# Kernel tuning notes

Hardware: AMD Instinct MI355X
Metric: run time of the kernel (lower is better)

The kernel has to match this reference:

```python
import jax, jax.numpy as jnp
import numpy as np

NEG_SLOPE = 0.01
H = 128  # hidden_conv_1 == hidden_conv_2


def leaky(x):
    return jnp.where(x >= 0, x, NEG_SLOPE * x)


def gru_cell(x, h, w_ih, w_hh, b_ih, b_hh):
    # PyTorch GRUCell: gates stacked [r, z, n] along dim 0 of w_ih/w_hh
    gi = x @ w_ih.T + b_ih  # [N, 3H]
    gh = h @ w_hh.T + b_hh
    ir, iz, inn = jnp.split(gi, 3, axis=-1)
    hr, hz, hn = jnp.split(gh, 3, axis=-1)
    r = jax.nn.sigmoid(ir + hr)
    z = jax.nn.sigmoid(iz + hz)
    n = jnp.tanh(inn + r * hn)
    return (1.0 - z) * n + z * h


def gcn_conv(x, w, b, src, dst, num_nodes):
    # PyG GCNConv: add self-loops, symmetric normalization, linear first
    xw = x @ w.T  # [N, H]
    loop = jnp.arange(num_nodes, dtype=src.dtype)
    s = jnp.concatenate([src, loop])
    d = jnp.concatenate([dst, loop])
    deg = jax.ops.segment_sum(jnp.ones_like(d, dtype=x.dtype), d, num_segments=num_nodes)
    dinv = jnp.where(deg > 0, jax.lax.rsqrt(deg), 0.0)
    norm = dinv[s] * dinv[d]  # [E+N]
    msg = xw[s] * norm[:, None]
    out = jax.ops.segment_sum(msg, d, num_segments=num_nodes)
    return out + b


def setup_inputs() -> dict:
    key = jax.random.key(0)
    ks = jax.random.split(key, 24)
    N, E, EL, IN_DIM, OUT_DIM = 100000, 600000, 200000, 128, 2

    def lin(k, fan_in, fan_out):
        k1, k2 = jax.random.split(k)
        bound = 1.0 / np.sqrt(fan_in)
        w = jax.random.uniform(k1, (fan_out, fan_in), minval=-bound, maxval=bound, dtype=jnp.float32)
        b = jax.random.uniform(k2, (fan_out,), minval=-bound, maxval=bound, dtype=jnp.float32)
        return w, b

    w_pre1, b_pre1 = lin(ks[0], IN_DIM, 256)
    w_pre2, b_pre2 = lin(ks[1], 256, H)
    w_c1, b_c1 = lin(ks[2], H, H)
    w_c2, b_c2 = lin(ks[3], H, H)
    w_post, b_post = lin(ks[4], H, OUT_DIM)

    def gru_params(k):
        k1, k2, k3, k4 = jax.random.split(k, 4)
        bound = 1.0 / np.sqrt(H)
        u = lambda kk, shape: jax.random.uniform(kk, shape, minval=-bound, maxval=bound, dtype=jnp.float32)
        return u(k1, (3 * H, H)), u(k2, (3 * H, H)), u(k3, (3 * H,)), u(k4, (3 * H,))

    g1_wih, g1_whh, g1_bih, g1_bhh = gru_params(ks[5])
    g2_wih, g2_whh, g2_bih, g2_bhh = gru_params(ks[6])

    x = jax.random.normal(ks[7], (N, IN_DIM), dtype=jnp.float32)
    edge_index = jax.random.randint(ks[8], (2, E), 0, N, dtype=jnp.int64 if jax.config.jax_enable_x64 else jnp.int32)
    edge_label_index = jax.random.randint(ks[9], (2, EL), 0, N, dtype=edge_index.dtype)
    prev_emb0 = jax.random.normal(ks[10], (N, H), dtype=jnp.float32)
    prev_emb1 = jax.random.normal(ks[11], (N, H), dtype=jnp.float32)

    return {
        'x': x, 'edge_index': edge_index, 'edge_label_index': edge_label_index,
        'prev_emb0': prev_emb0, 'prev_emb1': prev_emb1,
        'w_pre1': w_pre1, 'b_pre1': b_pre1, 'w_pre2': w_pre2, 'b_pre2': b_pre2,
        'w_c1': w_c1, 'b_c1': b_c1, 'w_c2': w_c2, 'b_c2': b_c2,
        'w_post': w_post, 'b_post': b_post,
        'g1_wih': g1_wih, 'g1_whh': g1_whh, 'g1_bih': g1_bih, 'g1_bhh': g1_bhh,
        'g2_wih': g2_wih, 'g2_whh': g2_whh, 'g2_bih': g2_bih, 'g2_bhh': g2_bhh,
    }


def reference(x, edge_index, edge_label_index, prev_emb0, prev_emb1,
              w_pre1, b_pre1, w_pre2, b_pre2, w_c1, b_c1, w_c2, b_c2,
              w_post, b_post, g1_wih, g1_whh, g1_bih, g1_bhh,
              g2_wih, g2_whh, g2_bih, g2_bhh):
    N = x.shape[0]
    src, dst = edge_index[0], edge_index[1]

    # preprocess (dropout p=0.0 -> identity)
    h = leaky(x @ w_pre1.T + b_pre1)
    h = leaky(h @ w_pre2.T + b_pre2)

    # unconditional GRU fuse with previous 0-hop embedding (detached in torch)
    h = jax.lax.stop_gradient(gru_cell(h, prev_emb0, g1_wih, g1_whh, g1_bih, g1_bhh))
    emb0 = h

    h = leaky(gcn_conv(h, w_c1, b_c1, src, dst, N))
    h = jax.lax.stop_gradient(gru_cell(h, prev_emb0, g1_wih, g1_whh, g1_bih, g1_bhh))
    emb1 = h

    h = leaky(gcn_conv(h, w_c2, b_c2, src, dst, N))
    h = jax.lax.stop_gradient(gru_cell(h, prev_emb1, g2_wih, g2_whh, g2_bih, g2_bhh))
    emb2 = h

    # LP head: gather + hadamard + linear + sum
    h_src = h[edge_label_index[0]]
    h_dst = h[edge_label_index[1]]
    logits = jnp.sum((h_src * h_dst) @ w_post.T + b_post, axis=-1)  # [EL]
    return logits, emb0, emb1, emb2
```

## Files before the change

### kernel.cpp

```cpp
#include <hip/hip_runtime.h>
#include <hip/hip_bf16.h>
#include <type_traits>


typedef __bf16 bf16;
typedef __bf16 bf16x8 __attribute__((ext_vector_type(8)));
typedef float  f32x4  __attribute__((ext_vector_type(4)));

#define DEV __device__ __forceinline__

DEV f32x4 mfma16(bf16x8 a, bf16x8 b, f32x4 c) {
    return __builtin_amdgcn_mfma_f32_16x16x32_bf16(a, b, c, 0, 0, 0);
}

DEV bf16x8 load_a8(const float* p) {
    f32x4 lo = *(const f32x4*)p;
    f32x4 hi = *(const f32x4*)(p + 4);
    bf16x8 v;
    v[0] = (bf16)lo[0]; v[1] = (bf16)lo[1]; v[2] = (bf16)lo[2]; v[3] = (bf16)lo[3];
    v[4] = (bf16)hi[0]; v[5] = (bf16)hi[1]; v[6] = (bf16)hi[2]; v[7] = (bf16)hi[3];
    return v;
}
DEV bf16x8 load_a8(const bf16* p) { return *(const bf16x8*)p; }

__global__ void cvt8_kernel(const float* s0, const float* s1, const float* s2, const float* s3,
                            const float* s4, const float* s5, const float* s6, const float* s7,
                            bf16* __restrict__ wb) {
    const int i = blockIdx.x * 256 + threadIdx.x;
    if (i >= 294912) return;
    float v;
    if      (i < 32768)  v = s0[i];
    else if (i < 65536)  v = s1[i - 32768];
    else if (i < 81920)  v = s2[i - 65536];
    else if (i < 98304)  v = s3[i - 81920];
    else if (i < 147456) v = s4[i - 98304];
    else if (i < 196608) v = s5[i - 147456];
    else if (i < 245760) v = s6[i - 196608];
    else                 v = s7[i - 245760];
    wb[i] = (bf16)v;
}

template<int Ci, int Co, bool ACT, bool BIAS, typename AT, typename OT>
__global__ __launch_bounds__(256) void gemm_kernel(
    const AT* __restrict__ A, const bf16* __restrict__ W,
    const float* __restrict__ bias, OT* __restrict__ C, int M)
{
    const int tid  = threadIdx.x;
    const int lane = tid & 63, w = tid >> 6;
    const int lr   = lane & 15, ko = lane >> 4;
    const int rbase = blockIdx.x * 128 + w * 32;

    constexpr int KC = Ci / 32;
    constexpr int NT = Co / 16;

    bf16x8 a[2][KC];
#pragma unroll
    for (int m = 0; m < 2; ++m) {
        long arow = rbase + m * 16 + lr; if (arow > M - 1) arow = M - 1;
#pragma unroll
        for (int kc = 0; kc < KC; ++kc)
            a[m][kc] = load_a8(A + arow * Ci + kc * 32 + ko * 8);
    }

#pragma unroll
    for (int t = 0; t < NT; ++t) {
        f32x4 acc0 = {0.f, 0.f, 0.f, 0.f};
        f32x4 acc1 = {0.f, 0.f, 0.f, 0.f};
        const bf16* wp = W + (long)(t * 16 + lr) * Ci + ko * 8;
#pragma unroll
        for (int kc = 0; kc < KC; ++kc) {
            bf16x8 wf = *(const bf16x8*)(wp + kc * 32);
            acc0 = mfma16(a[0][kc], wf, acc0);
            acc1 = mfma16(a[1][kc], wf, acc1);
        }

        const int col = t * 16 + lr;
        float bv = 0.f;
        if (BIAS) bv = bias[col];
#pragma unroll
        for (int j = 0; j < 4; ++j) {
            const int r0 = rbase + ko * 4 + j;
            if (r0 < M) {
                float v = acc0[j] + bv;
                if (ACT) v = (v >= 0.f) ? v : 0.01f * v;
                C[(long)r0 * Co + col] = (OT)v;
            }
            const int r1 = rbase + 16 + ko * 4 + j;
            if (r1 < M) {
                float v = acc1[j] + bv;
                if (ACT) v = (v >= 0.f) ? v : 0.01f * v;
                C[(long)r1 * Co + col] = (OT)v;
            }
        }
    }
}

template<typename XT>
__global__ __launch_bounds__(256) void gru_kernel(
    const XT* x, const float* __restrict__ hp,
    const bf16* __restrict__ wih, const bf16* __restrict__ whh,
    const float* __restrict__ bih, const float* __restrict__ bhh,
    float* out, int N)
{
    __shared__ bf16 Lw[6][16][128];

    const int tid  = threadIdx.x;
    const int lane = tid & 63, w = tid >> 6;
    const int lr   = lane & 15, ko = lane >> 4;
    const long rbase = (long)blockIdx.x * 64 + w * 16;

    long arow = rbase + lr; if (arow > N - 1) arow = N - 1;
    bf16x8 ax[4], ah[4];
#pragma unroll
    for (int kc = 0; kc < 4; ++kc) {
        ax[kc] = load_a8(x  + arow * 128 + kc * 32 + ko * 8);
        ah[kc] = load_a8(hp + arow * 128 + kc * 32 + ko * 8);
    }

    bf16x8 pre[6];
    auto LDW = [&](int tc) {
#pragma unroll
        for (int i = 0; i < 6; ++i) {
            const int ch  = tid + 256 * i;
            const int g   = ch >> 8, rem = ch & 255;
            const int row = rem >> 4, cc = rem & 15;
            const int scc = cc ^ (row & 7);
            pre[i] = *(const bf16x8*)((g < 3 ? wih : whh)
                + (long)(((g % 3) * 128 + tc * 16 + row) * 128 + scc * 8));
        }
    };
    LDW(0);

    for (int tc = 0; tc < 8; ++tc) {
        __syncthreads();
#pragma unroll
        for (int i = 0; i < 6; ++i) {
            const int ch  = tid + 256 * i;
            const int g   = ch >> 8, rem = ch & 255;
            const int row = rem >> 4, cc = rem & 15;
            *(bf16x8*)(&Lw[g][row][cc * 8]) = pre[i];
        }
        __syncthreads();
        if (tc < 7) LDW(tc + 1);

        const int col = tc * 16 + lr;
        const float br = bih[col]       + bhh[col];
        const float bz = bih[128 + col] + bhh[128 + col];
        const float bi = bih[256 + col];
        const float bh = bhh[256 + col];

        f32x4 ar = {0.f, 0.f, 0.f, 0.f};
        f32x4 az = {0.f, 0.f, 0.f, 0.f};
        f32x4 ai = {0.f, 0.f, 0.f, 0.f};
        f32x4 ag = {0.f, 0.f, 0.f, 0.f};
#pragma unroll
        for (int kc = 0; kc < 4; ++kc) {
            const int cc = (kc * 4 + ko) ^ (lr & 7);
            bf16x8 wr_i = *(const bf16x8*)(&Lw[0][lr][cc * 8]);
            bf16x8 wz_i = *(const bf16x8*)(&Lw[1][lr][cc * 8]);
            bf16x8 wn_i = *(const bf16x8*)(&Lw[2][lr][cc * 8]);
            bf16x8 wr_h = *(const bf16x8*)(&Lw[3][lr][cc * 8]);
            bf16x8 wz_h = *(const bf16x8*)(&Lw[4][lr][cc * 8]);
            bf16x8 wn_h = *(const bf16x8*)(&Lw[5][lr][cc * 8]);
            ar = mfma16(ax[kc], wr_i, ar);
            ar = mfma16(ah[kc], wr_h, ar);
            az = mfma16(ax[kc], wz_i, az);
            az = mfma16(ah[kc], wz_h, az);
            ai = mfma16(ax[kc], wn_i, ai);
            ag = mfma16(ah[kc], wn_h, ag);
        }
#pragma unroll
        for (int j = 0; j < 4; ++j) {
            const long row = rbase + ko * 4 + j;
            if (row < N) {
                const float r = 1.f / (1.f + __expf(-(ar[j] + br)));
                const float z = 1.f / (1.f + __expf(-(az[j] + bz)));
                const float pre_ = (ai[j] + bi) + r * (ag[j] + bh);
                const float n = 1.f - 2.f / (1.f + __expf(2.f * pre_));
                out[row * 128 + col] = (1.f - z) * n + z * hp[row * 128 + col];
            }
        }
    }
}

__global__ __launch_bounds__(256) void gg_kernel(
    const bf16* __restrict__ xwb,
    const int* __restrict__ rowptr, const int* __restrict__ degi,
    const int2* __restrict__ csr_pk,
    const float* __restrict__ dinv, const float* __restrict__ cbias,
    const float* __restrict__ hp,
    const bf16* __restrict__ wih, const bf16* __restrict__ whh,
    const float* __restrict__ bih, const float* __restrict__ bhh,
    float* __restrict__ out, int N)
{
    __shared__ bf16 Lw[6][16][128];

    const int tid  = threadIdx.x;
    const int lane = tid & 63, w = tid >> 6;
    const int lr   = lane & 15, ko = lane >> 4;
    const long rbase = (long)blockIdx.x * 64 + w * 16;

    long arow = rbase + lr; if (arow > N - 1) arow = N - 1;

    float acc[4][8];
#pragma unroll
    for (int kc = 0; kc < 4; ++kc)
#pragma unroll
        for (int j = 0; j < 8; ++j) acc[kc][j] = 0.f;
    {
        const int start = rowptr[arow];
        const int deg   = degi[arow];
        const bf16* xb  = xwb + ko * 8;
        int k = 0;
        for (; k + 2 <= deg; k += 2) {
            const int2 p0 = csr_pk[start + k];
            const int2 p1 = csr_pk[start + k + 1];
            const float nm0 = __int_as_float(p0.y);
            const float nm1 = __int_as_float(p1.y);
            const bf16* vp0 = xb + (long)p0.x * 128;
            const bf16* vp1 = xb + (long)p1.x * 128;
            bf16x8 a0 = *(const bf16x8*)(vp0);
            bf16x8 a1 = *(const bf16x8*)(vp0 + 32);
            bf16x8 a2 = *(const bf16x8*)(vp0 + 64);
            bf16x8 a3 = *(const bf16x8*)(vp0 + 96);
            bf16x8 b0 = *(const bf16x8*)(vp1);
            bf16x8 b1 = *(const bf16x8*)(vp1 + 32);
            bf16x8 b2 = *(const bf16x8*)(vp1 + 64);
            bf16x8 b3 = *(const bf16x8*)(vp1 + 96);
#pragma unroll
            for (int j = 0; j < 8; ++j) {
                acc[0][j] += (float)a0[j] * nm0 + (float)b0[j] * nm1;
                acc[1][j] += (float)a1[j] * nm0 + (float)b1[j] * nm1;
                acc[2][j] += (float)a2[j] * nm0 + (float)b2[j] * nm1;
                acc[3][j] += (float)a3[j] * nm0 + (float)b3[j] * nm1;
            }
        }
        if (k < deg) {
            const int2 p0 = csr_pk[start + k];
            const float nm0 = __int_as_float(p0.y);
            const bf16* vp0 = xb + (long)p0.x * 128;
            bf16x8 a0 = *(const bf16x8*)(vp0);
            bf16x8 a1 = *(const bf16x8*)(vp0 + 32);
            bf16x8 a2 = *(const bf16x8*)(vp0 + 64);
            bf16x8 a3 = *(const bf16x8*)(vp0 + 96);
#pragma unroll
            for (int j = 0; j < 8; ++j) {
                acc[0][j] += (float)a0[j] * nm0;
                acc[1][j] += (float)a1[j] * nm0;
                acc[2][j] += (float)a2[j] * nm0;
                acc[3][j] += (float)a3[j] * nm0;
            }
        }
    }

    bf16x8 ax[4], ah[4];
    {
        const float di = dinv[arow], sl = di * di;
        const bf16* vp = xwb + (long)arow * 128 + ko * 8;
#pragma unroll
        for (int kc = 0; kc < 4; ++kc) {
            bf16x8 vd = *(const bf16x8*)(vp + kc * 32);
#pragma unroll
            for (int j = 0; j < 8; ++j) {
                float t = acc[kc][j] + (float)vd[j] * sl + cbias[kc * 32 + ko * 8 + j];
                t = (t >= 0.f) ? t : 0.01f * t;
                ax[kc][j] = (bf16)t;
            }
            ah[kc] = load_a8(hp + arow * 128 + kc * 32 + ko * 8);
        }
    }

    bf16x8 pre[6];
    auto LDW = [&](int tc) {
#pragma unroll
        for (int i = 0; i < 6; ++i) {
            const int ch  = tid + 256 * i;
            const int g   = ch >> 8, rem = ch & 255;
            const int row = rem >> 4, cc = rem & 15;
            const int scc = cc ^ (row & 7);
            pre[i] = *(const bf16x8*)((g < 3 ? wih : whh)
                + (long)(((g % 3) * 128 + tc * 16 + row) * 128 + scc * 8));
        }
    };
    LDW(0);

    for (int tc = 0; tc < 8; ++tc) {
        __syncthreads();
#pragma unroll
        for (int i = 0; i < 6; ++i) {
            const int ch  = tid + 256 * i;
            const int g   = ch >> 8, rem = ch & 255;
            const int row = rem >> 4, cc = rem & 15;
            *(bf16x8*)(&Lw[g][row][cc * 8]) = pre[i];
        }
        __syncthreads();
        if (tc < 7) LDW(tc + 1);

        const int col = tc * 16 + lr;
        const float br = bih[col]       + bhh[col];
        const float bz = bih[128 + col] + bhh[128 + col];
        const float bi = bih[256 + col];
        const float bh = bhh[256 + col];

        f32x4 ar = {0.f, 0.f, 0.f, 0.f};
        f32x4 az = {0.f, 0.f, 0.f, 0.f};
        f32x4 ai = {0.f, 0.f, 0.f, 0.f};
        f32x4 ag = {0.f, 0.f, 0.f, 0.f};
        __builtin_amdgcn_s_setprio(1);
#pragma unroll
        for (int kc = 0; kc < 4; ++kc) {
            const int cc = (kc * 4 + ko) ^ (lr & 7);
            bf16x8 wr_i = *(const bf16x8*)(&Lw[0][lr][cc * 8]);
            bf16x8 wz_i = *(const bf16x8*)(&Lw[1][lr][cc * 8]);
            bf16x8 wn_i = *(const bf16x8*)(&Lw[2][lr][cc * 8]);
            bf16x8 wr_h = *(const bf16x8*)(&Lw[3][lr][cc * 8]);
            bf16x8 wz_h = *(const bf16x8*)(&Lw[4][lr][cc * 8]);
            bf16x8 wn_h = *(const bf16x8*)(&Lw[5][lr][cc * 8]);
            ar = mfma16(ax[kc], wr_i, ar);
            ar = mfma16(ah[kc], wr_h, ar);
            az = mfma16(ax[kc], wz_i, az);
            az = mfma16(ah[kc], wz_h, az);
            ai = mfma16(ax[kc], wn_i, ai);
            ag = mfma16(ah[kc], wn_h, ag);
        }
        __builtin_amdgcn_s_setprio(0);
#pragma unroll
        for (int j = 0; j < 4; ++j) {
            const long row = rbase + ko * 4 + j;
            if (row < N) {
                const float r = 1.f / (1.f + __expf(-(ar[j] + br)));
                const float z = 1.f / (1.f + __expf(-(az[j] + bz)));
                const float pre_ = (ai[j] + bi) + r * (ag[j] + bh);
                const float n = 1.f - 2.f / (1.f + __expf(2.f * pre_));
                out[row * 128 + col] = (1.f - z) * n + z * hp[row * 128 + col];
            }
        }
    }
}

__global__ void deg_kernel(const int* __restrict__ dst, int* degi, int E) {
    const int e = blockIdx.x * 256 + threadIdx.x;
    if (e < E) atomicAdd(&degi[dst[e]], 1);
}
__global__ void scan1_kernel(const int* __restrict__ degi, int* __restrict__ inc,
                             int* __restrict__ bsum, float* __restrict__ dinv, int N) {
    __shared__ int s[256];
    const int i = blockIdx.x * 256 + threadIdx.x;
    const int d = (i < N) ? degi[i] : 0;
    if (i < N) dinv[i] = rsqrtf((float)d + 1.0f);
    s[threadIdx.x] = d;
    __syncthreads();
#pragma unroll
    for (int off = 1; off < 256; off <<= 1) {
        int t = (threadIdx.x >= off) ? s[threadIdx.x - off] : 0;
        __syncthreads();
        s[threadIdx.x] += t;
        __syncthreads();
    }
    if (i < N) inc[i] = s[threadIdx.x];
    if (threadIdx.x == 255) bsum[blockIdx.x] = s[255];
}
__global__ void scan2_kernel(int* bsum, int nb) {
    __shared__ int s[512];
    __shared__ int carry;
    if (threadIdx.x == 0) carry = 0;
    __syncthreads();
    for (int base = 0; base < nb; base += 512) {
        const int i = base + threadIdx.x;
        s[threadIdx.x] = (i < nb) ? bsum[i] : 0;
        __syncthreads();
#pragma unroll
        for (int off = 1; off < 512; off <<= 1) {
            int t = (threadIdx.x >= off) ? s[threadIdx.x - off] : 0;
            __syncthreads();
            s[threadIdx.x] += t;
            __syncthreads();
        }
        const int c = carry;
        if (i < nb) bsum[i] = s[threadIdx.x] + c;
        __syncthreads();
        if (threadIdx.x == 511) carry = c + s[511];
        __syncthreads();
    }
}
__global__ void scan3_kernel(const int* __restrict__ inc, const int* __restrict__ degi,
                             const int* __restrict__ bsum, int* __restrict__ rowptr,
                             int* __restrict__ rp2, int N) {
    const int i = blockIdx.x * 256 + threadIdx.x;
    if (i >= N) return;
    const int prev = (blockIdx.x > 0) ? bsum[blockIdx.x - 1] : 0;
    const int rp = prev + inc[i] - degi[i];
    rowptr[i] = rp;
    rp2[i]    = rp;
}
__global__ void fill_kernel(const int* __restrict__ src, const int* __restrict__ dst,
                            int* rp2, const float* __restrict__ dinv,
                            int* __restrict__ csr_src, float* __restrict__ csr_norm,
                            int2* __restrict__ csr_pk, int E) {
    const int e = blockIdx.x * 256 + threadIdx.x;
    if (e >= E) return;
    const int s = src[e], d = dst[e];
    const int pos = atomicAdd(&rp2[d], 1);
    const float nm = dinv[s] * dinv[d];
    csr_src[pos]  = s;
    csr_norm[pos] = nm;
    csr_pk[pos]   = make_int2(s, __float_as_int(nm));
}

template<typename OT>
__global__ __launch_bounds__(256) void gather_kernel(
    const bf16* __restrict__ xwb,
    const int* __restrict__ rowptr, const int* __restrict__ degi,
    const int* __restrict__ csr_src, const float* __restrict__ csr_norm,
    const float* __restrict__ dinv, const float* __restrict__ bias,
    OT* __restrict__ out, int N, int colbase, int cw, int lg)
{
    const long tid = (long)blockIdx.x * 256 + threadIdx.x;
    const long d = tid >> lg;
    const int  c = (int)(tid & ((1 << lg) - 1));
    if (d >= N) return;

    const int start = rowptr[d];
    const int deg   = degi[d];
    const int h     = deg >> 1;
    const bf16* xb  = xwb + c * 8;

    float acca[8] = {0.f, 0.f, 0.f, 0.f, 0.f, 0.f, 0.f, 0.f};
    float accb[8] = {0.f, 0.f, 0.f, 0.f, 0.f, 0.f, 0.f, 0.f};
    for (int k = 0; k < h; ++k) {
        const int   sa = csr_src[start + k];
        const int   sb = csr_src[start + h + k];
        const float na = csr_norm[start + k];
        const float nb_ = csr_norm[start + h + k];
        bf16x8 va = *(const bf16x8*)(xb + (long)sa * cw);
        bf16x8 vb = *(const bf16x8*)(xb + (long)sb * cw);
#pragma unroll
        for (int j = 0; j < 8; ++j) {
            acca[j] += (float)va[j] * na;
            accb[j] += (float)vb[j] * nb_;
        }
    }
    if (deg & 1) {
        const int   s  = csr_src[start + deg - 1];
        const float nm = csr_norm[start + deg - 1];
        bf16x8 v = *(const bf16x8*)(xb + (long)s * cw);
#pragma unroll
        for (int j = 0; j < 8; ++j) acca[j] += (float)v[j] * nm;
    }

    const float di = dinv[d], sl = di * di;
    bf16x8 vd = *(const bf16x8*)(xb + d * cw);
    const int col = colbase + c * 8;
    float v[8];
#pragma unroll
    for (int j = 0; j < 8; ++j) {
        float t = acca[j] + accb[j] + (float)vd[j] * sl + bias[col + j];
        v[j] = (t >= 0.f) ? t : 0.01f * t;
    }
    if constexpr (std::is_same<OT, bf16>::value) {
        bf16x8 o;
#pragma unroll
        for (int j = 0; j < 8; ++j) o[j] = (bf16)v[j];
        *(bf16x8*)(out + d * 128 + col) = o;
    } else {
        f32x4 o0, o1;
#pragma unroll
        for (int j = 0; j < 4; ++j) { o0[j] = v[j]; o1[j] = v[4 + j]; }
        *(f32x4*)(out + d * 128 + col)     = o0;
        *(f32x4*)(out + d * 128 + col + 4) = o1;
    }
}

__global__ __launch_bounds__(256) void lp_kernel(
    const float* __restrict__ emb, const int* __restrict__ eli,
    const float* __restrict__ wpost, const float* __restrict__ bpost,
    float* __restrict__ logits, int EL)
{
    const long t = (long)blockIdx.x * 256 + threadIdx.x;
    const long e = t >> 4;
    const int  c = (int)(t & 15);
    if (e >= EL) return;
    const long s = eli[e], d = eli[EL + e];

    f32x4 a0 = *(const f32x4*)(emb + s * 128 + c * 8);
    f32x4 a1 = *(const f32x4*)(emb + s * 128 + c * 8 + 4);
    f32x4 b0 = *(const f32x4*)(emb + d * 128 + c * 8);
    f32x4 b1 = *(const f32x4*)(emb + d * 128 + c * 8 + 4);
    f32x4 w00 = *(const f32x4*)(wpost + c * 8);
    f32x4 w01 = *(const f32x4*)(wpost + c * 8 + 4);
    f32x4 w10 = *(const f32x4*)(wpost + 128 + c * 8);
    f32x4 w11 = *(const f32x4*)(wpost + 128 + c * 8 + 4);

    float acc = 0.f;
#pragma unroll
    for (int i = 0; i < 4; ++i) {
        acc += a0[i] * b0[i] * (w00[i] + w10[i]);
        acc += a1[i] * b1[i] * (w01[i] + w11[i]);
    }
#pragma unroll
    for (int m = 1; m < 16; m <<= 1) acc += __shfl_xor(acc, m);
    if (c == 0) logits[e] = acc + bpost[0] + bpost[1];
}

extern "C" void kernel_launch(void* const* d_in, const int* in_sizes, int n_in,
                              void* d_out, int out_size, void* d_ws, size_t ws_size,
                              hipStream_t stream) {
    const float* x      = (const float*)d_in[0];
    const int*   ei     = (const int*)d_in[1];
    const int*   eli    = (const int*)d_in[2];
    const float* prev0  = (const float*)d_in[3];
    const float* prev1  = (const float*)d_in[4];
    const float* w_pre1 = (const float*)d_in[5];
    const float* b_pre1 = (const float*)d_in[6];
    const float* w_pre2 = (const float*)d_in[7];
    const float* b_pre2 = (const float*)d_in[8];
    const float* w_c1   = (const float*)d_in[9];
    const float* b_c1   = (const float*)d_in[10];
    const float* w_c2   = (const float*)d_in[11];
    const float* b_c2   = (const float*)d_in[12];
    const float* w_post = (const float*)d_in[13];
    const float* b_post = (const float*)d_in[14];
    const float* g1_wih = (const float*)d_in[15];
    const float* g1_whh = (const float*)d_in[16];
    const float* g1_bih = (const float*)d_in[17];
    const float* g1_bhh = (const float*)d_in[18];
    const float* g2_wih = (const float*)d_in[19];
    const float* g2_whh = (const float*)d_in[20];
    const float* g2_bih = (const float*)d_in[21];
    const float* g2_bhh = (const float*)d_in[22];

    const int N  = in_sizes[0] / 128;
    const int E  = in_sizes[1] / 2;
    const int EL = in_sizes[2] / 2;
    const long NH = (long)N * 128;

    float* out    = (float*)d_out;
    float* logits = out;
    float* emb0   = out + EL;
    float* emb1   = emb0 + NH;
    float* emb2   = emb1 + NH;

    bf16* H1b = (bf16*)emb1;
    bf16* H2b = (bf16*)emb2;
    bf16* h1b = (bf16*)emb2;

    char* ws = (char*)d_ws;
    size_t p = 0;
    auto alloc = [&](size_t bytes) { size_t o = p; p = (p + bytes + 255) & ~(size_t)255; return o; };
    float* dinv    = (float*)(ws + alloc((size_t)N * 4));
    int*   degi    = (int*)  (ws + alloc((size_t)N * 4));
    int*   inc     = (int*)  (ws + alloc((size_t)N * 4));
    int*   rowptr  = (int*)  (ws + alloc((size_t)(N + 1) * 4));
    int*   rp2     = (int*)  (ws + alloc((size_t)N * 4));
    int*   bsum    = (int*)  (ws + alloc(4096));
    bf16*  wb      = (bf16*) (ws + alloc((size_t)294912 * 2));
    int*   csr_src = (int*)  (ws + alloc((size_t)E * 4));
    float* csr_nrm = (float*)(ws + alloc((size_t)E * 4));
    int2*  csr_pk  = (int2*) (ws + alloc((size_t)E * 8));
    const size_t fixed = p;
    bf16*  xwb     = (bf16*)(ws + fixed);

    int cw = 128;
    while (cw > 16 && fixed + (size_t)N * cw * 2 > ws_size) cw >>= 1;
    const int lg = __builtin_ctz(cw >> 3);
    const int passes = 128 / cw;
    const bool fused = (cw == 128);
    const bool big_ws = fused &&
        (ws_size >= fixed + (size_t)N * 128 * 2 + (size_t)N * 128 * 2);
    bf16* h2b = big_ws ? (bf16*)(ws + fixed + (size_t)N * 128 * 2) : nullptr;

    bf16* wb_pre1 = wb;
    bf16* wb_pre2 = wb_pre1 + 32768;
    bf16* wb_c1   = wb_pre2 + 32768;
    bf16* wb_c2   = wb_c1 + 16384;
    bf16* wb_g1i  = wb_c2 + 16384;
    bf16* wb_g1h  = wb_g1i + 49152;
    bf16* wb_g2i  = wb_g1h + 49152;
    bf16* wb_g2h  = wb_g2i + 49152;

    const int gB = 256;
    const dim3 blk(gB);
    const int grid_rows128 = (N + 127) / 128;
    const int grid_gru     = (N + 63) / 64;
    const int grid_E       = (E + gB - 1) / gB;
    const int nb           = (N + 255) / 256;

    cvt8_kernel<<<(294912 + 255) / 256, blk, 0, stream>>>(
        w_pre1, w_pre2, w_c1, w_c2, g1_wih, g1_whh, g2_wih, g2_whh, wb);

    hipMemsetAsync(degi, 0, (size_t)N * 4, stream);
    deg_kernel<<<grid_E, blk, 0, stream>>>(ei + E, degi, E);
    scan1_kernel<<<nb, blk, 0, stream>>>(degi, inc, bsum, dinv, N);
    scan2_kernel<<<1, 512, 0, stream>>>(bsum, nb);
    scan3_kernel<<<nb, blk, 0, stream>>>(inc, degi, bsum, rowptr, rp2, N);
    fill_kernel<<<grid_E, blk, 0, stream>>>(ei, ei + E, rp2, dinv, csr_src, csr_nrm, csr_pk, E);

    gemm_kernel<128, 256, true, true, float, bf16><<<grid_rows128, blk, 0, stream>>>(x, wb_pre1, b_pre1, H1b, N);
    gemm_kernel<256, 128, true, true, bf16,  bf16><<<grid_rows128, blk, 0, stream>>>(H1b, wb_pre2, b_pre2, H2b, N);

    gru_kernel<bf16><<<grid_gru, blk, 0, stream>>>(H2b, prev0, wb_g1i, wb_g1h, g1_bih, g1_bhh, emb0, N);

    auto run_gemm = [&](const float* hin, const bf16* wp) {
        switch (cw) {
        case 128: gemm_kernel<128, 128, false, false, float, bf16><<<grid_rows128, blk, 0, stream>>>(hin, wp, nullptr, xwb, N); break;
        case 64:  gemm_kernel<128, 64,  false, false, float, bf16><<<grid_rows128, blk, 0, stream>>>(hin, wp, nullptr, xwb, N); break;
        case 32:  gemm_kernel<128, 32,  false, false, float, bf16><<<grid_rows128, blk, 0, stream>>>(hin, wp, nullptr, xwb, N); break;
        default:  gemm_kernel<128, 16,  false, false, float, bf16><<<grid_rows128, blk, 0, stream>>>(hin, wp, nullptr, xwb, N); break;
        }
    };

    if (fused) {
        run_gemm(emb0, wb_c1);
        gg_kernel<<<grid_gru, blk, 0, stream>>>(xwb, rowptr, degi, csr_pk,
                                                dinv, b_c1, prev0,
                                                wb_g1i, wb_g1h, g1_bih, g1_bhh, emb1, N);
        run_gemm(emb1, wb_c2);
        gg_kernel<<<grid_gru, blk, 0, stream>>>(xwb, rowptr, degi, csr_pk,
                                                dinv, b_c2, prev1,
                                                wb_g2i, wb_g2h, g2_bih, g2_bhh, emb2, N);
    } else {
        const int grid_ga = (int)((((long)N << lg) + gB - 1) / gB);
        for (int ps = 0; ps < passes; ++ps) {
            run_gemm(emb0, wb_c1 + (size_t)(ps * cw) * 128);
            gather_kernel<bf16><<<grid_ga, blk, 0, stream>>>(xwb, rowptr, degi, csr_src, csr_nrm,
                                                             dinv, b_c1, h1b, N, ps * cw, cw, lg);
        }
        gru_kernel<bf16><<<grid_gru, blk, 0, stream>>>(h1b, prev0, wb_g1i, wb_g1h, g1_bih, g1_bhh, emb1, N);
        for (int ps = 0; ps < passes; ++ps) {
            run_gemm(emb1, wb_c2 + (size_t)(ps * cw) * 128);
            if (big_ws)
                gather_kernel<bf16><<<grid_ga, blk, 0, stream>>>(xwb, rowptr, degi, csr_src, csr_nrm,
                                                                 dinv, b_c2, h2b, N, ps * cw, cw, lg);
            else
                gather_kernel<float><<<grid_ga, blk, 0, stream>>>(xwb, rowptr, degi, csr_src, csr_nrm,
                                                                  dinv, b_c2, emb2, N, ps * cw, cw, lg);
        }
        if (big_ws)
            gru_kernel<bf16><<<grid_gru, blk, 0, stream>>>(h2b, prev1, wb_g2i, wb_g2h, g2_bih, g2_bhh, emb2, N);
        else
            gru_kernel<float><<<grid_gru, blk, 0, stream>>>(emb2, prev1, wb_g2i, wb_g2h, g2_bih, g2_bhh, emb2, N);
    }

    lp_kernel<<<(int)(((long)EL * 16 + gB - 1) / gB), blk, 0, stream>>>(emb2, eli, w_post, b_post, logits, EL);
}
```

Baseline: 528.4 us.

## Sort nodes by degree so fused gather-GRU waves get balanced work

Adds a histogram, scan and scatter pass that builds a permutation of nodes grouped by in-degree (capped at 63). The fused gather+GRU kernel then processes rows in this permuted order, so the 16 rows sharing a wave have similar degrees and less lane divergence in the neighbor loop. It also drops the separate csr_src/csr_norm arrays and has the unfused gather path read the packed int2 CSR. The cost is three extra small kernels plus scattered row reads and writes of hp and out through perm, which loses locality.

```diff
diff --git a/kernel.cpp b/kernel.cpp
--- a/kernel.cpp
+++ b/kernel.cpp
@@ -186,7 +186,7 @@
 __global__ __launch_bounds__(256) void gg_kernel(
     const bf16* __restrict__ xwb,
     const int* __restrict__ rowptr, const int* __restrict__ degi,
-    const int2* __restrict__ csr_pk,
+    const int2* __restrict__ csr_pk, const int* __restrict__ perm,
     const float* __restrict__ dinv, const float* __restrict__ cbias,
     const float* __restrict__ hp,
     const bf16* __restrict__ wih, const bf16* __restrict__ whh,
@@ -194,13 +194,21 @@
     float* __restrict__ out, int N)
 {
     __shared__ bf16 Lw[6][16][128];
+    __shared__ int  sperm[64];
 
     const int tid  = threadIdx.x;
     const int lane = tid & 63, w = tid >> 6;
     const int lr   = lane & 15, ko = lane >> 4;
-    const long rbase = (long)blockIdx.x * 64 + w * 16;
-
-    long arow = rbase + lr; if (arow > N - 1) arow = N - 1;
+    const long rbase = (long)blockIdx.x * 64;
+    const long wrow0 = rbase + w * 16;
+
+    if (tid < 64) {
+        long ii = rbase + tid; if (ii > N - 1) ii = N - 1;
+        sperm[tid] = perm[ii];
+    }
+    __syncthreads();
+
+    const long arow = sperm[w * 16 + lr];
 
     float acc[4][8];
 #pragma unroll
@@ -326,8 +334,8 @@
         __builtin_amdgcn_s_setprio(0);
 #pragma unroll
         for (int j = 0; j < 4; ++j) {
-            const long row = rbase + ko * 4 + j;
-            if (row < N) {
+            if (wrow0 + ko * 4 + j < N) {
+                const long row = sperm[w * 16 + ko * 4 + j];
                 const float r = 1.f / (1.f + __expf(-(ar[j] + br)));
                 const float z = 1.f / (1.f + __expf(-(az[j] + bz)));
                 const float pre_ = (ai[j] + bi) + r * (ag[j] + bh);
@@ -395,23 +403,68 @@
 }
 __global__ void fill_kernel(const int* __restrict__ src, const int* __restrict__ dst,
                             int* rp2, const float* __restrict__ dinv,
-                            int* __restrict__ csr_src, float* __restrict__ csr_norm,
                             int2* __restrict__ csr_pk, int E) {
     const int e = blockIdx.x * 256 + threadIdx.x;
     if (e >= E) return;
     const int s = src[e], d = dst[e];
     const int pos = atomicAdd(&rp2[d], 1);
-    const float nm = dinv[s] * dinv[d];
-    csr_src[pos]  = s;
-    csr_norm[pos] = nm;
-    csr_pk[pos]   = make_int2(s, __float_as_int(nm));
+    csr_pk[pos] = make_int2(s, __float_as_int(dinv[s] * dinv[d]));
+}
+
+__global__ void bhist_kernel(const int* __restrict__ degi, int* __restrict__ binof,
+                             int* __restrict__ rankin, int* __restrict__ bh,
+                             int N, int nbB) {
+    __shared__ int h[64];
+    const int i = blockIdx.x * 256 + threadIdx.x;
+    if (threadIdx.x < 64) h[threadIdx.x] = 0;
+    __syncthreads();
+    if (i < N) {
+        int b = degi[i]; if (b > 63) b = 63;
+        const int r = atomicAdd(&h[b], 1);
+        binof[i]  = b;
+        rankin[i] = r;
+    }
+    __syncthreads();
+    if (threadIdx.x < 64) bh[threadIdx.x * nbB + blockIdx.x] = h[threadIdx.x];
+}
+__global__ void gscan_kernel(int* bh, int total) {
+    __shared__ int ssum[256];
+    const int t = threadIdx.x;
+    const int seg = (total + 255) / 256;
+    const int s0 = t * seg;
+    const int s1 = (s0 + seg < total) ? (s0 + seg) : total;
+    int sum = 0;
+    for (int i = s0; i < s1; ++i) sum += bh[i];
+    ssum[t] = sum;
+    __syncthreads();
+#pragma unroll
+    for (int off = 1; off < 256; off <<= 1) {
+        int v = (t >= off) ? ssum[t - off] : 0;
+        __syncthreads();
+        ssum[t] += v;
+        __syncthreads();
+    }
+    int run = ssum[t] - sum;
+    for (int i = s0; i < s1; ++i) {
+        const int v = bh[i];
+        bh[i] = run;
+        run += v;
+    }
+}
+__global__ void pscatter_kernel(const int* __restrict__ binof, const int* __restrict__ rankin,
+                                const int* __restrict__ bh, int* __restrict__ perm,
+                                int N, int nbB) {
+    const int i = blockIdx.x * 256 + threadIdx.x;
+    if (i >= N) return;
+    const int pos = bh[binof[i] * nbB + blockIdx.x] + rankin[i];
+    perm[pos] = i;
 }
 
 template<typename OT>
 __global__ __launch_bounds__(256) void gather_kernel(
     const bf16* __restrict__ xwb,
     const int* __restrict__ rowptr, const int* __restrict__ degi,
-    const int* __restrict__ csr_src, const float* __restrict__ csr_norm,
+    const int2* __restrict__ csr_pk,
     const float* __restrict__ dinv, const float* __restrict__ bias,
     OT* __restrict__ out, int N, int colbase, int cw, int lg)
 {
@@ -428,12 +481,12 @@
     float acca[8] = {0.f, 0.f, 0.f, 0.f, 0.f, 0.f, 0.f, 0.f};
     float accb[8] = {0.f, 0.f, 0.f, 0.f, 0.f, 0.f, 0.f, 0.f};
     for (int k = 0; k < h; ++k) {
-        const int   sa = csr_src[start + k];
-        const int   sb = csr_src[start + h + k];
-        const float na = csr_norm[start + k];
-        const float nb_ = csr_norm[start + h + k];
-        bf16x8 va = *(const bf16x8*)(xb + (long)sa * cw);
-        bf16x8 vb = *(const bf16x8*)(xb + (long)sb * cw);
+        const int2 pa = csr_pk[start + k];
+        const int2 pb = csr_pk[start + h + k];
+        bf16x8 va = *(const bf16x8*)(xb + (long)pa.x * cw);
+        bf16x8 vb = *(const bf16x8*)(xb + (long)pb.x * cw);
+        const float na  = __int_as_float(pa.y);
+        const float nb_ = __int_as_float(pb.y);
 #pragma unroll
         for (int j = 0; j < 8; ++j) {
             acca[j] += (float)va[j] * na;
@@ -441,9 +494,9 @@
         }
     }
     if (deg & 1) {
-        const int   s  = csr_src[start + deg - 1];
-        const float nm = csr_norm[start + deg - 1];
-        bf16x8 v = *(const bf16x8*)(xb + (long)s * cw);
+        const int2 pa = csr_pk[start + deg - 1];
+        const float nm = __int_as_float(pa.y);
+        bf16x8 v = *(const bf16x8*)(xb + (long)pa.x * cw);
 #pragma unroll
         for (int j = 0; j < 8; ++j) acca[j] += (float)v[j] * nm;
     }
@@ -547,15 +600,18 @@
     char* ws = (char*)d_ws;
     size_t p = 0;
     auto alloc = [&](size_t bytes) { size_t o = p; p = (p + bytes + 255) & ~(size_t)255; return o; };
+    const int nbB = (N + 255) / 256;
     float* dinv    = (float*)(ws + alloc((size_t)N * 4));
     int*   degi    = (int*)  (ws + alloc((size_t)N * 4));
     int*   inc     = (int*)  (ws + alloc((size_t)N * 4));
     int*   rowptr  = (int*)  (ws + alloc((size_t)(N + 1) * 4));
     int*   rp2     = (int*)  (ws + alloc((size_t)N * 4));
     int*   bsum    = (int*)  (ws + alloc(4096));
+    int*   binof   = (int*)  (ws + alloc((size_t)N * 4));
+    int*   rankin  = (int*)  (ws + alloc((size_t)N * 4));
+    int*   bh      = (int*)  (ws + alloc((size_t)64 * nbB * 4));
+    int*   perm    = (int*)  (ws + alloc((size_t)N * 4));
     bf16*  wb      = (bf16*) (ws + alloc((size_t)294912 * 2));
-    int*   csr_src = (int*)  (ws + alloc((size_t)E * 4));
-    float* csr_nrm = (float*)(ws + alloc((size_t)E * 4));
     int2*  csr_pk  = (int2*) (ws + alloc((size_t)E * 8));
     const size_t fixed = p;
     bf16*  xwb     = (bf16*)(ws + fixed);
@@ -583,17 +639,19 @@
     const int grid_rows128 = (N + 127) / 128;
     const int grid_gru     = (N + 63) / 64;
     const int grid_E       = (E + gB - 1) / gB;
-    const int nb           = (N + 255) / 256;
 
     cvt8_kernel<<<(294912 + 255) / 256, blk, 0, stream>>>(
         w_pre1, w_pre2, w_c1, w_c2, g1_wih, g1_whh, g2_wih, g2_whh, wb);
 
     hipMemsetAsync(degi, 0, (size_t)N * 4, stream);
     deg_kernel<<<grid_E, blk, 0, stream>>>(ei + E, degi, E);
-    scan1_kernel<<<nb, blk, 0, stream>>>(degi, inc, bsum, dinv, N);
-    scan2_kernel<<<1, 512, 0, stream>>>(bsum, nb);
-    scan3_kernel<<<nb, blk, 0, stream>>>(inc, degi, bsum, rowptr, rp2, N);
-    fill_kernel<<<grid_E, blk, 0, stream>>>(ei, ei + E, rp2, dinv, csr_src, csr_nrm, csr_pk, E);
+    scan1_kernel<<<nbB, blk, 0, stream>>>(degi, inc, bsum, dinv, N);
+    scan2_kernel<<<1, 512, 0, stream>>>(bsum, nbB);
+    scan3_kernel<<<nbB, blk, 0, stream>>>(inc, degi, bsum, rowptr, rp2, N);
+    fill_kernel<<<grid_E, blk, 0, stream>>>(ei, ei + E, rp2, dinv, csr_pk, E);
+    bhist_kernel<<<nbB, blk, 0, stream>>>(degi, binof, rankin, bh, N, nbB);
+    gscan_kernel<<<1, blk, 0, stream>>>(bh, 64 * nbB);
+    pscatter_kernel<<<nbB, blk, 0, stream>>>(binof, rankin, bh, perm, N, nbB);
 
     gemm_kernel<128, 256, true, true, float, bf16><<<grid_rows128, blk, 0, stream>>>(x, wb_pre1, b_pre1, H1b, N);
     gemm_kernel<256, 128, true, true, bf16,  bf16><<<grid_rows128, blk, 0, stream>>>(H1b, wb_pre2, b_pre2, H2b, N);
@@ -611,28 +669,28 @@
 
     if (fused) {
         run_gemm(emb0, wb_c1);
-        gg_kernel<<<grid_gru, blk, 0, stream>>>(xwb, rowptr, degi, csr_pk,
+        gg_kernel<<<grid_gru, blk, 0, stream>>>(xwb, rowptr, degi, csr_pk, perm,
                                                 dinv, b_c1, prev0,
                                                 wb_g1i, wb_g1h, g1_bih, g1_bhh, emb1, N);
         run_gemm(emb1, wb_c2);
-        gg_kernel<<<grid_gru, blk, 0, stream>>>(xwb, rowptr, degi, csr_pk,
+        gg_kernel<<<grid_gru, blk, 0, stream>>>(xwb, rowptr, degi, csr_pk, perm,
                                                 dinv, b_c2, prev1,
                                                 wb_g2i, wb_g2h, g2_bih, g2_bhh, emb2, N);
     } else {
         const int grid_ga = (int)((((long)N << lg) + gB - 1) / gB);
         for (int ps = 0; ps < passes; ++ps) {
             run_gemm(emb0, wb_c1 + (size_t)(ps * cw) * 128);
-            gather_kernel<bf16><<<grid_ga, blk, 0, stream>>>(xwb, rowptr, degi, csr_src, csr_nrm,
+            gather_kernel<bf16><<<grid_ga, blk, 0, stream>>>(xwb, rowptr, degi, csr_pk,
                                                              dinv, b_c1, h1b, N, ps * cw, cw, lg);
         }
         gru_kernel<bf16><<<grid_gru, blk, 0, stream>>>(h1b, prev0, wb_g1i, wb_g1h, g1_bih, g1_bhh, emb1, N);
         for (int ps = 0; ps < passes; ++ps) {
             run_gemm(emb1, wb_c2 + (size_t)(ps * cw) * 128);
             if (big_ws)
-                gather_kernel<bf16><<<grid_ga, blk, 0, stream>>>(xwb, rowptr, degi, csr_src, csr_nrm,
+                gather_kernel<bf16><<<grid_ga, blk, 0, stream>>>(xwb, rowptr, degi, csr_pk,
                                                                  dinv, b_c2, h2b, N, ps * cw, cw, lg);
             else
-                gather_kernel<float><<<grid_ga, blk, 0, stream>>>(xwb, rowptr, degi, csr_src, csr_nrm,
+                gather_kernel<float><<<grid_ga, blk, 0, stream>>>(xwb, rowptr, degi, csr_pk,
                                                                   dinv, b_c2, emb2, N, ps * cw, cw, lg);
         }
         if (big_ws)
```

New measurement: 574.7 us. 8.8% more time.
